# Kernel optimization log

Hardware: AMD Instinct MI355X
Metric: run time of the kernel (lower is better)

The kernel has to match this reference:

```python
import jax, jax.numpy as jnp
import numpy as np

N, D_IN = 40000, 3000
E = 640000
ALPHA = 0.9
BN_EPS = 0.001      # nn.BatchNorm in encoder/decoder blocks (eps=0.001)
BN_EPS_CONV = 1e-5  # PyG BatchNorm default eps
NEG_SLOPE = 0.2     # GATConv leaky_relu slope


def _bn(x, g, b, m, v, eps):
    # inference-mode batchnorm with running stats
    return (x - m) * (g / jnp.sqrt(v + eps)) + b


def _gat(h, src, dst, W, a_src, a_dst, bias, n):
    # PyG GATConv (heads=1): linear transform, per-edge additive attention,
    # segment softmax over incoming edges (self-loops already in src/dst).
    hw = h @ W                                   # [n, out]
    s_src = (hw * a_src).sum(-1)                 # [n]
    s_dst = (hw * a_dst).sum(-1)                 # [n]
    al = jax.nn.leaky_relu(s_src[src] + s_dst[dst], NEG_SLOPE)  # [e]
    mx = jax.ops.segment_max(al, dst, num_segments=n)
    e = jnp.exp(al - mx[dst])
    z = jax.ops.segment_sum(e, dst, num_segments=n)
    w = e / (z[dst] + 1e-16)                     # softmax weight per edge
    out = jax.ops.segment_sum(w[:, None] * hw[src], dst, num_segments=n)
    return out + bias


def _forward(x, edge_index,
             e0_w, e0_b, e0_g, e0_beta, e0_m, e0_v,
             e1_w, e1_b, e1_g, e1_beta, e1_m, e1_v,
             g1_w, g1_as, g1_ad, g1_b, bnc_g, bnc_beta, bnc_m, bnc_v,
             gm_w, gm_as, gm_ad, gm_b,
             gv_w, gv_as, gv_ad, gv_b,
             d0_w, d0_b, d0_g, d0_beta, d0_m, d0_v,
             out_w, out_b, cluster, eps):
    ar = jnp.arange(N, dtype=edge_index.dtype)
    src = jnp.concatenate([edge_index[0], ar])   # add self-loops (GATConv default)
    dst = jnp.concatenate([edge_index[1], ar])

    # linear encoder: Linear -> BN -> ELU (dropout inactive at eval)
    h = jax.nn.elu(_bn(x @ e0_w + e0_b, e0_g, e0_beta, e0_m, e0_v, BN_EPS))
    feat_x = jax.nn.elu(_bn(h @ e1_w + e1_b, e1_g, e1_beta, e1_m, e1_v, BN_EPS))

    # graph conv stack
    c = _gat(feat_x, src, dst, g1_w, g1_as, g1_ad, g1_b, N)
    c = jax.nn.relu(_bn(c, bnc_g, bnc_beta, bnc_m, bnc_v, BN_EPS_CONV))
    mu = _gat(c, src, dst, gm_w, gm_as, gm_ad, gm_b, N)
    logvar = _gat(c, src, dst, gv_w, gv_as, gv_ad, gv_b, N)

    # reparameterize (std = exp(logvar) per original code)
    gnn_z = eps * jnp.exp(logvar) + mu
    z = jnp.concatenate([feat_x, gnn_z], axis=1)  # [N, 28]

    # linear decoder
    d = jax.nn.elu(_bn(z @ d0_w + d0_b, d0_g, d0_beta, d0_m, d0_v, BN_EPS))
    de_feat = d @ out_w + out_b                   # [N, D_IN]

    # DEC student-t soft assignment (squared distance via expansion)
    sq = jnp.maximum(
        jnp.sum(z * z, 1)[:, None] + jnp.sum(cluster * cluster, 1)[None, :]
        - 2.0 * (z @ cluster.T), 0.0)             # [N, K]
    q = 1.0 / (1.0 + sq / ALPHA + 1e-8)
    q = q ** ((ALPHA + 1.0) / 2.0)
    q = q / jnp.sum(q, 1, keepdims=True)
    return z, mu, logvar, de_feat, q, feat_x, gnn_z


def setup_inputs() -> dict:
    key = jax.random.key(0)
    ks = iter(jax.random.split(key, 48))
    nrm = lambda shape, s=0.1: jax.random.normal(next(ks), shape, jnp.float32) * s
    pos = lambda shape: jax.random.uniform(next(ks), shape, jnp.float32, 0.5, 1.5)
    inp = {}
    inp['x'] = jax.random.normal(next(ks), (N, D_IN), jnp.float32)
    inp['edge_index'] = jax.random.randint(next(ks), (2, E), 0, N, jnp.int32)
    # encoder L0: 3000 -> 32
    inp.update(e0_w=nrm((D_IN, 32), 0.02), e0_b=nrm((32,)), e0_g=pos((32,)),
               e0_beta=nrm((32,)), e0_m=nrm((32,)), e0_v=pos((32,)))
    # encoder L1: 32 -> 20
    inp.update(e1_w=nrm((32, 20)), e1_b=nrm((20,)), e1_g=pos((20,)),
               e1_beta=nrm((20,)), e1_m=nrm((20,)), e1_v=pos((20,)))
    # GATConv 20 -> 64 (+ PyG BatchNorm)
    inp.update(g1_w=nrm((20, 64)), g1_as=nrm((64,)), g1_ad=nrm((64,)), g1_b=nrm((64,)),
               bnc_g=pos((64,)), bnc_beta=nrm((64,)), bnc_m=nrm((64,)), bnc_v=pos((64,)))
    # GATConv mean / logvar: 64 -> 8
    inp.update(gm_w=nrm((64, 8)), gm_as=nrm((8,)), gm_ad=nrm((8,)), gm_b=nrm((8,)))
    inp.update(gv_w=nrm((64, 8)), gv_as=nrm((8,)), gv_ad=nrm((8,)), gv_b=nrm((8,)))
    # decoder L0: 28 -> 32, out: 32 -> 3000
    inp.update(d0_w=nrm((28, 32)), d0_b=nrm((32,)), d0_g=pos((32,)),
               d0_beta=nrm((32,)), d0_m=nrm((32,)), d0_v=pos((32,)))
    inp.update(out_w=nrm((32, D_IN), 0.05), out_b=nrm((D_IN,)))
    inp['cluster'] = nrm((15, 28), 0.5)
    inp['eps'] = jax.random.normal(next(ks), (N, 8), jnp.float32)
    return inp


def reference(x, edge_index,
              e0_w, e0_b, e0_g, e0_beta, e0_m, e0_v,
              e1_w, e1_b, e1_g, e1_beta, e1_m, e1_v,
              g1_w, g1_as, g1_ad, g1_b, bnc_g, bnc_beta, bnc_m, bnc_v,
              gm_w, gm_as, gm_ad, gm_b,
              gv_w, gv_as, gv_ad, gv_b,
              d0_w, d0_b, d0_g, d0_beta, d0_m, d0_v,
              out_w, out_b, cluster, eps):
    return _forward(x, edge_index,
                    e0_w, e0_b, e0_g, e0_beta, e0_m, e0_v,
                    e1_w, e1_b, e1_g, e1_beta, e1_m, e1_v,
                    g1_w, g1_as, g1_ad, g1_b, bnc_g, bnc_beta, bnc_m, bnc_v,
                    gm_w, gm_as, gm_ad, gm_b,
                    gv_w, gv_as, gv_ad, gv_b,
                    d0_w, d0_b, d0_g, d0_beta, d0_m, d0_v,
                    out_w, out_b, cluster, eps)
```

## Files before the change

kernel.cpp:

```cpp
#include <hip/hip_runtime.h>
#include <cfloat>
#include <cmath>

#define NN 40000
#define DIN 3000
#define NE 640000
#define ET (NE + NN)

#define NKS 94
#define NKH 47
#define NCT 192
#define NB_E 2657
#define DCAP 64

typedef __attribute__((ext_vector_type(8))) short short8;
typedef __attribute__((ext_vector_type(4))) float f32x4;

union frag16 { short8 s; uint4 u; };

__device__ __forceinline__ float lrelu(float x) { return x >= 0.f ? x : 0.2f * x; }
__device__ __forceinline__ float elu(float x)   { return x > 0.f ? x : expm1f(x); }
__device__ __forceinline__ unsigned f2bf(float f) {
    unsigned u = __float_as_uint(f);
    return (u + 0x7FFFu + ((u >> 16) & 1u)) >> 16;
}
__device__ __forceinline__ float bf2f(unsigned short us) {
    return __uint_as_float((unsigned)us << 16);
}

__global__ void k_fill_prep(const int* __restrict__ ei, int* __restrict__ cnt,
                            int* __restrict__ srcs,
                            const float* __restrict__ w, const float* __restrict__ ow,
                            unsigned short* __restrict__ bfw,
                            unsigned short* __restrict__ bfragb)
{
    if (blockIdx.x < NB_E) {
        int e = blockIdx.x * 256 + threadIdx.x;
        if (e >= ET) return;
        int s, d;
        if (e < NE) { s = ei[e]; d = ei[NE + e]; } else { s = d = e - NE; }
        int pos = atomicAdd(&cnt[d], 1);
        if (pos < DCAP) srcs[((size_t)d << 6) + pos] = s;
    } else {
        int id = (blockIdx.x - NB_E) * 256 + threadIdx.x;
        if (id < 96 * 128) {
            int ks = id >> 7, r = id & 127;
            int t = r >> 6, l = r & 63;
            int col = t * 16 + (l & 15);
            int k0 = ks * 32 + ((l >> 4) << 3);
            unsigned v[8];
            #pragma unroll
            for (int j = 0; j < 8; j++) {
                int k = k0 + j;
                v[j] = (k < DIN) ? f2bf(w[(size_t)k * 32 + col]) : 0u;
            }
            uint4 p;
            p.x = v[0] | (v[1] << 16); p.y = v[2] | (v[3] << 16);
            p.z = v[4] | (v[5] << 16); p.w = v[6] | (v[7] << 16);
            *(uint4*)&bfw[(size_t)id * 8] = p;
        } else {
            int tt = id - 96 * 128;
            if (tt < NCT * 64) {
                int ct = tt >> 6, l = tt & 63;
                int col = ct * 16 + (l & 15);
                int k0 = (l >> 4) * 8;
                uint4 p = make_uint4(0u, 0u, 0u, 0u);
                if (col < DIN) {
                    unsigned v[8];
                    #pragma unroll
                    for (int j = 0; j < 8; j++)
                        v[j] = f2bf(ow[(size_t)(k0 + j) * DIN + col]);
                    p.x = v[0] | (v[1] << 16); p.y = v[2] | (v[3] << 16);
                    p.z = v[4] | (v[5] << 16); p.w = v[6] | (v[7] << 16);
                }
                *(uint4*)&bfragb[((size_t)ct * 64 + l) * 8] = p;
            }
        }
    }
}

__global__ __launch_bounds__(128) void k_enc0_prep(
    const float* __restrict__ x, const unsigned short* __restrict__ bfw,
    const float* __restrict__ b, const float* __restrict__ g,
    const float* __restrict__ beta, const float* __restrict__ m,
    const float* __restrict__ v,
    const float* __restrict__ e1w, const float* __restrict__ e1b,
    const float* __restrict__ e1g, const float* __restrict__ e1beta,
    const float* __restrict__ e1m, const float* __restrict__ e1v,
    const float* __restrict__ g1w, const float* __restrict__ g1as,
    const float* __restrict__ g1ad,
    float* __restrict__ out_fx, unsigned short* __restrict__ hw1b,
    float* __restrict__ s1src, float* __restrict__ s1dst)
{
    __shared__ float red[64 * 8];
    __shared__ float hs[16][33];
    __shared__ float fxs[16][20];
    const int tid = threadIdx.x, wid = tid >> 6, l = tid & 63;
    const int gg = blockIdx.x;
    const int row0 = gg * 16;
    const int row = row0 + (l & 15);
    const int klane = (l >> 4) << 3;

    const float* xp = x + (size_t)row * DIN + klane;
    const unsigned short* bp = bfw + (size_t)l * 8;

    f32x4 acc0 = {0.f, 0.f, 0.f, 0.f};
    f32x4 acc1 = {0.f, 0.f, 0.f, 0.f};

    const int ks0 = wid * NKH;
    #pragma unroll 4
    for (int ks = ks0; ks < ks0 + NKH; ks++) {
        frag16 a; a.u = make_uint4(0u, 0u, 0u, 0u);
        int k = ks * 32 + klane;
        if (k < DIN) {
            float4 v0 = *(const float4*)(xp + ks * 32);
            float4 v1 = *(const float4*)(xp + ks * 32 + 4);
            a.u.x = f2bf(v0.x) | (f2bf(v0.y) << 16);
            a.u.y = f2bf(v0.z) | (f2bf(v0.w) << 16);
            a.u.z = f2bf(v1.x) | (f2bf(v1.y) << 16);
            a.u.w = f2bf(v1.z) | (f2bf(v1.w) << 16);
        }
        frag16 b0, b1;
        b0.u = *(const uint4*)(bp + (size_t)(ks * 2 + 0) * 512);
        b1.u = *(const uint4*)(bp + (size_t)(ks * 2 + 1) * 512);
        acc0 = __builtin_amdgcn_mfma_f32_16x16x32_bf16(a.s, b0.s, acc0, 0, 0, 0);
        acc1 = __builtin_amdgcn_mfma_f32_16x16x32_bf16(a.s, b1.s, acc1, 0, 0, 0);
    }

    if (wid == 1) {
        #pragma unroll
        for (int r = 0; r < 4; r++) {
            red[l * 8 + r]     = acc0[r];
            red[l * 8 + 4 + r] = acc1[r];
        }
    }
    __syncthreads();
    if (wid == 0) {
        #pragma unroll
        for (int r = 0; r < 4; r++) {
            acc0[r] += red[l * 8 + r];
            acc1[r] += red[l * 8 + 4 + r];
        }
        const int cl = l & 15;
        const int rloc = (l >> 4) * 4;
        float sc0 = g[cl] * rsqrtf(v[cl] + 1e-3f);
        float sh0 = beta[cl] - m[cl] * sc0;
        float bb0 = b[cl];
        float sc1 = g[cl + 16] * rsqrtf(v[cl + 16] + 1e-3f);
        float sh1 = beta[cl + 16] - m[cl + 16] * sc1;
        float bb1 = b[cl + 16];
        #pragma unroll
        for (int reg = 0; reg < 4; reg++) {
            hs[rloc + reg][cl]      = elu((acc0[reg] + bb0) * sc0 + sh0);
            hs[rloc + reg][cl + 16] = elu((acc1[reg] + bb1) * sc1 + sh1);
        }
    }
    __syncthreads();

    for (int i = tid; i < 320; i += 128) {
        int r = i / 20, c = i - r * 20;
        float s = e1b[c];
        #pragma unroll
        for (int k = 0; k < 32; k++) s += hs[r][k] * e1w[k * 20 + c];
        float sc = e1g[c] * rsqrtf(e1v[c] + 1e-3f);
        s = (s - e1m[c]) * sc + e1beta[c];
        float fx = elu(s);
        fxs[r][c] = fx;
        out_fx[(size_t)(row0 + r) * 20 + c] = fx;
    }
    __syncthreads();

    #pragma unroll
    for (int j = 0; j < 8; j++) {
        const int rl = 2 * j + wid;
        float s = 0.f;
        #pragma unroll
        for (int k = 0; k < 20; k++) s += fxs[rl][k] * g1w[k * 64 + l];
        hw1b[(size_t)(row0 + rl) * 64 + l] = (unsigned short)f2bf(s);
        float u1 = s * g1as[l];
        float u2 = s * g1ad[l];
        u1 += __shfl_xor(u1, 1); u1 += __shfl_xor(u1, 2); u1 += __shfl_xor(u1, 4);
        u1 += __shfl_xor(u1, 8); u1 += __shfl_xor(u1, 16); u1 += __shfl_xor(u1, 32);
        u2 += __shfl_xor(u2, 1); u2 += __shfl_xor(u2, 2); u2 += __shfl_xor(u2, 4);
        u2 += __shfl_xor(u2, 8); u2 += __shfl_xor(u2, 16); u2 += __shfl_xor(u2, 32);
        if (l == 0) { s1src[row0 + rl] = u1; s1dst[row0 + rl] = u2; }
    }
}

__global__ __launch_bounds__(256) void k_gat1_fused(
    const int* __restrict__ cnt, const int* __restrict__ srcs,
    const float* __restrict__ s1src, const float* __restrict__ s1dst,
    const unsigned short* __restrict__ hw1b,
    const float* __restrict__ g1b,
    const float* __restrict__ bncg, const float* __restrict__ bncbeta,
    const float* __restrict__ bncm, const float* __restrict__ bncv,
    const float* __restrict__ gmw, const float* __restrict__ gmas, const float* __restrict__ gmad,
    const float* __restrict__ gvw, const float* __restrict__ gvas, const float* __restrict__ gvad,
    float* __restrict__ hwmv, float* __restrict__ sv4)
{
    __shared__ float cs[4][64];
    const int wv = threadIdx.x >> 6;
    int d = (blockIdx.x * 256 + threadIdx.x) >> 6;
    int l = threadIdx.x & 63;
    if (d >= NN) return;
    const int j0 = d << 6;
    int n = cnt[d]; n = (n < DCAP) ? n : DCAP;
    float sd = s1dst[d];
    float acc = 0.f, z = 0.f;
    int j = 0;
    for (; j + 4 <= n; j += 4) {
        int s0 = srcs[j0 + j], s1 = srcs[j0 + j + 1];
        int s2 = srcs[j0 + j + 2], s3 = srcs[j0 + j + 3];
        float a0 = s1src[s0], a1 = s1src[s1], a2 = s1src[s2], a3 = s1src[s3];
        float h0 = bf2f(hw1b[(size_t)s0 * 64 + l]);
        float h1 = bf2f(hw1b[(size_t)s1 * 64 + l]);
        float h2 = bf2f(hw1b[(size_t)s2 * 64 + l]);
        float h3 = bf2f(hw1b[(size_t)s3 * 64 + l]);
        float e0 = expf(lrelu(a0 + sd)), e1 = expf(lrelu(a1 + sd));
        float e2 = expf(lrelu(a2 + sd)), e3 = expf(lrelu(a3 + sd));
        z += (e0 + e1) + (e2 + e3);
        acc += e0 * h0; acc += e1 * h1; acc += e2 * h2; acc += e3 * h3;
    }
    for (; j < n; j++) {
        int s = srcs[j0 + j];
        float ex = expf(lrelu(s1src[s] + sd));
        z += ex;
        acc += ex * bf2f(hw1b[(size_t)s * 64 + l]);
    }
    float zi = 1.f / (z + 1e-16f);
    float val = acc * zi + g1b[l];
    float sc = bncg[l] * rsqrtf(bncv[l] + 1e-5f);
    val = (val - bncm[l]) * sc + bncbeta[l];
    float c = val > 0.f ? val : 0.f;
    cs[wv][l] = c;

    if (l < 16) {
        const bool isv = l >= 8;
        const int o = l & 7;
        const float* wmat = isv ? gvw : gmw;
        float s = 0.f;
        #pragma unroll 8
        for (int k = 0; k < 64; k++)
            s += cs[wv][k] * wmat[k * 8 + o];
        hwmv[(size_t)d * 16 + l] = s;
        float u1 = s * (isv ? gvas[o] : gmas[o]);
        float u2 = s * (isv ? gvad[o] : gmad[o]);
        u1 += __shfl_xor(u1, 1); u1 += __shfl_xor(u1, 2); u1 += __shfl_xor(u1, 4);
        u2 += __shfl_xor(u2, 1); u2 += __shfl_xor(u2, 2); u2 += __shfl_xor(u2, 4);
        if (o == 0) {
            if (!isv) { sv4[(size_t)d * 4 + 0] = u1; sv4[(size_t)d * 4 + 1] = u2; }
            else      { sv4[(size_t)d * 4 + 2] = u1; sv4[(size_t)d * 4 + 3] = u2; }
        }
    }
}

__global__ __launch_bounds__(256) void k_gat23_final(
    const int* __restrict__ cnt, const int* __restrict__ srcs,
    const float* __restrict__ hwmv, const float* __restrict__ sv4,
    const float* __restrict__ gmb, const float* __restrict__ gvb,
    const float* __restrict__ epsin, const float* __restrict__ fx_out,
    const float* __restrict__ d0w, const float* __restrict__ d0b,
    const float* __restrict__ d0g, const float* __restrict__ d0beta,
    const float* __restrict__ d0m, const float* __restrict__ d0v,
    const float* __restrict__ cluster,
    float* __restrict__ out_z, float* __restrict__ out_mu, float* __restrict__ out_lv,
    float* __restrict__ out_q, float* __restrict__ out_gz,
    unsigned short* __restrict__ abuf)
{
    __shared__ float zs[4][28];
    __shared__ float dvs[4][32];
    const int wv = threadIdx.x >> 6;
    int d = (blockIdx.x * 256 + threadIdx.x) >> 6;
    int l = threadIdx.x & 63;
    if (d >= NN) return;
    const int eg = l >> 4;
    const bool isv = (l & 15) >= 8;
    const int f = l & 7;
    const int fmv = l & 15;
    const int j0 = d << 6;
    int n = cnt[d]; n = (n < DCAP) ? n : DCAP;
    float sdst = sv4[(size_t)d * 4 + (isv ? 3 : 1)];
    float acc = 0.f, z = 0.f;
    for (int j = eg; j < n; j += 4) {
        int s = srcs[j0 + j];
        float a = sv4[(size_t)s * 4 + (isv ? 2 : 0)] + sdst;
        float ex = expf(lrelu(a));
        z += ex;
        acc += ex * hwmv[(size_t)s * 16 + fmv];
    }
    acc += __shfl_xor(acc, 16); acc += __shfl_xor(acc, 32);
    z   += __shfl_xor(z, 16);   z   += __shfl_xor(z, 32);
    float zi = 1.f / (z + 1e-16f);
    float t = acc * zi + (isv ? gvb[f] : gmb[f]);
    float partner = __shfl_xor(t, 8);
    float gz = 0.f;
    if (l < 8) gz = epsin[(size_t)d * 8 + f] * expf(partner) + t;
    if (l < 8)        { out_mu[(size_t)d * 8 + f] = t; out_gz[(size_t)d * 8 + f] = gz; }
    else if (l < 16)  { out_lv[(size_t)d * 8 + f] = t; }
    if (l < 20) zs[wv][l] = fx_out[(size_t)d * 20 + l];
    if (l < 8)  zs[wv][20 + l] = gz;
    if (l < 28) out_z[(size_t)d * 28 + l] = zs[wv][l];
    if (l < 32) {
        float s = d0b[l];
        #pragma unroll
        for (int k = 0; k < 28; k++) s += zs[wv][k] * d0w[k * 32 + l];
        float sc = d0g[l] * rsqrtf(d0v[l] + 1e-3f);
        s = (s - d0m[l]) * sc + d0beta[l];
        dvs[wv][l] = elu(s);
    }
    if (l < 4) {
        int g = d >> 4, rl = d & 15;
        const float* dv = dvs[wv];
        uint4 p;
        p.x = f2bf(dv[l*8+0]) | (f2bf(dv[l*8+1]) << 16);
        p.y = f2bf(dv[l*8+2]) | (f2bf(dv[l*8+3]) << 16);
        p.z = f2bf(dv[l*8+4]) | (f2bf(dv[l*8+5]) << 16);
        p.w = f2bf(dv[l*8+6]) | (f2bf(dv[l*8+7]) << 16);
        *(uint4*)&abuf[(size_t)g * 512 + (rl + 16 * l) * 8] = p;
    }
    float zz = 0.f;
    #pragma unroll
    for (int k = 0; k < 28; k++) { float zk = zs[wv][k]; zz += zk * zk; }
    float qb = 0.f;
    if (l < 15) {
        float cc = 0.f, zc = 0.f;
        #pragma unroll
        for (int k = 0; k < 28; k++) {
            float cv = cluster[l * 28 + k];
            cc += cv * cv; zc += zs[wv][k] * cv;
        }
        float sq = zz + cc - 2.f * zc;
        if (sq < 0.f) sq = 0.f;
        qb = 1.f / (1.f + sq * (1.f / 0.9f) + 1e-8f);
        qb = powf(qb, 0.95f);
    }
    float qs = qb;
    qs += __shfl_xor(qs, 1); qs += __shfl_xor(qs, 2);
    qs += __shfl_xor(qs, 4); qs += __shfl_xor(qs, 8);
    if (l < 15) out_q[(size_t)d * 15 + l] = qb / qs;
}

#define OTS 132
__global__ __launch_bounds__(256) void k_dec_out(
    const unsigned short* __restrict__ abuf, const unsigned short* __restrict__ bfragb,
    const float* __restrict__ ob, float* __restrict__ out_de)
{
    __shared__ float ot[64 * OTS];
    const int tid = threadIdx.x, wid = tid >> 6, l = tid & 63;
    const int gblk = blockIdx.y;
    const int ct0 = blockIdx.x * 8;
    frag16 a; a.u = *(const uint4*)&abuf[((size_t)(gblk * 4 + wid)) * 512 + l * 8];
    const int lrow = wid * 16 + (l >> 4) * 4;
    const int cl = l & 15;
    #pragma unroll
    for (int c = 0; c < 8; c++) {
        frag16 bfr; bfr.u = *(const uint4*)&bfragb[((size_t)(ct0 + c) * 64 + l) * 8];
        f32x4 acc = {0.f, 0.f, 0.f, 0.f};
        acc = __builtin_amdgcn_mfma_f32_16x16x32_bf16(a.s, bfr.s, acc, 0, 0, 0);
        #pragma unroll
        for (int reg = 0; reg < 4; reg++)
            ot[(lrow + reg) * OTS + c * 16 + cl] = acc[reg];
    }
    __syncthreads();
    const int row0 = gblk * 64;
    const int c0 = ct0 * 16;
    #pragma unroll
    for (int i = 0; i < 8; i++) {
        int idx = i * 256 + tid;
        int r = idx >> 5, q = idx & 31;
        int col = c0 + q * 4;
        if (col < DIN) {
            const float* p = &ot[r * OTS + q * 4];
            float4 bq = *(const float4*)&ob[col];
            f32x4 o;
            o[0] = p[0] + bq.x; o[1] = p[1] + bq.y;
            o[2] = p[2] + bq.z; o[3] = p[3] + bq.w;
            __builtin_nontemporal_store(o, (f32x4*)&out_de[(size_t)(row0 + r) * DIN + col]);
        }
    }
}

extern "C" void kernel_launch(void* const* d_in, const int* in_sizes, int n_in,
                              void* d_out, int out_size, void* d_ws, size_t ws_size,
                              hipStream_t stream) {
    const float* x      = (const float*)d_in[0];
    const int*   ei     = (const int*)  d_in[1];
    const float* e0_w   = (const float*)d_in[2];
    const float* e0_b   = (const float*)d_in[3];
    const float* e0_g   = (const float*)d_in[4];
    const float* e0_be  = (const float*)d_in[5];
    const float* e0_m   = (const float*)d_in[6];
    const float* e0_v   = (const float*)d_in[7];
    const float* e1_w   = (const float*)d_in[8];
    const float* e1_b   = (const float*)d_in[9];
    const float* e1_g   = (const float*)d_in[10];
    const float* e1_be  = (const float*)d_in[11];
    const float* e1_m   = (const float*)d_in[12];
    const float* e1_v   = (const float*)d_in[13];
    const float* g1_w   = (const float*)d_in[14];
    const float* g1_as  = (const float*)d_in[15];
    const float* g1_ad  = (const float*)d_in[16];
    const float* g1_b   = (const float*)d_in[17];
    const float* bnc_g  = (const float*)d_in[18];
    const float* bnc_be = (const float*)d_in[19];
    const float* bnc_m  = (const float*)d_in[20];
    const float* bnc_v  = (const float*)d_in[21];
    const float* gm_w   = (const float*)d_in[22];
    const float* gm_as  = (const float*)d_in[23];
    const float* gm_ad  = (const float*)d_in[24];
    const float* gm_b   = (const float*)d_in[25];
    const float* gv_w   = (const float*)d_in[26];
    const float* gv_as  = (const float*)d_in[27];
    const float* gv_ad  = (const float*)d_in[28];
    const float* gv_b   = (const float*)d_in[29];
    const float* d0_w   = (const float*)d_in[30];
    const float* d0_b   = (const float*)d_in[31];
    const float* d0_g   = (const float*)d_in[32];
    const float* d0_be  = (const float*)d_in[33];
    const float* d0_m   = (const float*)d_in[34];
    const float* d0_v   = (const float*)d_in[35];
    const float* out_w  = (const float*)d_in[36];
    const float* out_b  = (const float*)d_in[37];
    const float* cluster= (const float*)d_in[38];
    const float* epsin  = (const float*)d_in[39];

    float* out = (float*)d_out;
    float* out_z  = out;
    float* out_mu = out + (size_t)NN * 28;
    float* out_lv = out + (size_t)NN * 36;
    float* out_de = out + (size_t)NN * 44;
    float* out_q  = out + (size_t)NN * 44 + (size_t)NN * DIN;
    float* out_fx = out + (size_t)NN * 59 + (size_t)NN * DIN;
    float* out_gz = out + (size_t)NN * 79 + (size_t)NN * DIN;

    float* ws = (float*)d_ws;
    const size_t n = NN;
    unsigned short* hw1b = (unsigned short*)(ws + 64 * n);
    float* s1src   = ws + 96 * n;
    float* s1dst   = ws + 97 * n;
    unsigned short* abuf   = (unsigned short*)(ws + 103 * n);
    unsigned short* bfw    = (unsigned short*)(ws + 119 * n);
    unsigned short* bfragb = (unsigned short*)(ws + 121 * n);
    float* hwmv = ws;
    float* sv4  = ws + 16 * n;

    int* srcs = (int*)out_de;
    int* cnt  = srcs + (size_t)NN * DCAP;

    const int NB_PREP = (96 * 128 + NCT * 64 + 255) / 256;

    (void)hipMemsetAsync(cnt, 0, NN * sizeof(int), stream);
    k_fill_prep<<<NB_E + NB_PREP, 256, 0, stream>>>(ei, cnt, srcs, e0_w, out_w, bfw, bfragb);

    k_enc0_prep<<<NN / 16, 128, 0, stream>>>(x, bfw, e0_b, e0_g, e0_be, e0_m, e0_v,
                                             e1_w, e1_b, e1_g, e1_be, e1_m, e1_v,
                                             g1_w, g1_as, g1_ad,
                                             out_fx, hw1b, s1src, s1dst);
    k_gat1_fused<<<(NN * 64 + 255) / 256, 256, 0, stream>>>(cnt, srcs,
                                                            s1src, s1dst, hw1b,
                                                            g1_b, bnc_g, bnc_be, bnc_m, bnc_v,
                                                            gm_w, gm_as, gm_ad,
                                                            gv_w, gv_as, gv_ad,
                                                            hwmv, sv4);
    k_gat23_final<<<(NN * 64 + 255) / 256, 256, 0, stream>>>(cnt, srcs,
                                                             hwmv, sv4,
                                                             gm_b, gv_b, epsin, out_fx,
                                                             d0_w, d0_b, d0_g, d0_be, d0_m, d0_v,
                                                             cluster,
                                                             out_z, out_mu, out_lv, out_q, out_gz,
                                                             abuf);
    dim3 dec_grid(NCT / 8, NN / 64);
    k_dec_out<<<dec_grid, 256, 0, stream>>>(abuf, bfragb, out_b, out_de);
}
```

Baseline: 433.0 us.

## Move edge bucketing into encoder kernel to overlap with the GEMM

The edge-to-destination bucketing (atomic count plus source scatter) moves out of the weight-prep kernel and into the front of the encoder GEMM kernel's grid, using extra blocks. The weight-prep kernel now only converts weights to bf16 fragments and launches far fewer blocks. The aim is to run the latency-bound atomic scatter alongside the bandwidth-bound x@W encoder instead of serially before it. The extra scatter blocks are dispatched first and could delay the GEMM blocks.

```diff
diff --git a/kernel.cpp b/kernel.cpp
--- a/kernel.cpp
+++ b/kernel.cpp
@@ -28,53 +28,42 @@
     return __uint_as_float((unsigned)us << 16);
 }
 
-__global__ void k_fill_prep(const int* __restrict__ ei, int* __restrict__ cnt,
-                            int* __restrict__ srcs,
-                            const float* __restrict__ w, const float* __restrict__ ow,
-                            unsigned short* __restrict__ bfw,
-                            unsigned short* __restrict__ bfragb)
+__global__ void k_wprep(const float* __restrict__ w, const float* __restrict__ ow,
+                        unsigned short* __restrict__ bfw,
+                        unsigned short* __restrict__ bfragb)
 {
-    if (blockIdx.x < NB_E) {
-        int e = blockIdx.x * 256 + threadIdx.x;
-        if (e >= ET) return;
-        int s, d;
-        if (e < NE) { s = ei[e]; d = ei[NE + e]; } else { s = d = e - NE; }
-        int pos = atomicAdd(&cnt[d], 1);
-        if (pos < DCAP) srcs[((size_t)d << 6) + pos] = s;
+    int id = blockIdx.x * 256 + threadIdx.x;
+    if (id < 96 * 128) {
+        int ks = id >> 7, r = id & 127;
+        int t = r >> 6, l = r & 63;
+        int col = t * 16 + (l & 15);
+        int k0 = ks * 32 + ((l >> 4) << 3);
+        unsigned v[8];
+        #pragma unroll
+        for (int j = 0; j < 8; j++) {
+            int k = k0 + j;
+            v[j] = (k < DIN) ? f2bf(w[(size_t)k * 32 + col]) : 0u;
+        }
+        uint4 p;
+        p.x = v[0] | (v[1] << 16); p.y = v[2] | (v[3] << 16);
+        p.z = v[4] | (v[5] << 16); p.w = v[6] | (v[7] << 16);
+        *(uint4*)&bfw[(size_t)id * 8] = p;
     } else {
-        int id = (blockIdx.x - NB_E) * 256 + threadIdx.x;
-        if (id < 96 * 128) {
-            int ks = id >> 7, r = id & 127;
-            int t = r >> 6, l = r & 63;
-            int col = t * 16 + (l & 15);
-            int k0 = ks * 32 + ((l >> 4) << 3);
-            unsigned v[8];
-            #pragma unroll
-            for (int j = 0; j < 8; j++) {
-                int k = k0 + j;
-                v[j] = (k < DIN) ? f2bf(w[(size_t)k * 32 + col]) : 0u;
+        int tt = id - 96 * 128;
+        if (tt < NCT * 64) {
+            int ct = tt >> 6, l = tt & 63;
+            int col = ct * 16 + (l & 15);
+            int k0 = (l >> 4) * 8;
+            uint4 p = make_uint4(0u, 0u, 0u, 0u);
+            if (col < DIN) {
+                unsigned v[8];
+                #pragma unroll
+                for (int j = 0; j < 8; j++)
+                    v[j] = f2bf(ow[(size_t)(k0 + j) * DIN + col]);
+                p.x = v[0] | (v[1] << 16); p.y = v[2] | (v[3] << 16);
+                p.z = v[4] | (v[5] << 16); p.w = v[6] | (v[7] << 16);
             }
-            uint4 p;
-            p.x = v[0] | (v[1] << 16); p.y = v[2] | (v[3] << 16);
-            p.z = v[4] | (v[5] << 16); p.w = v[6] | (v[7] << 16);
-            *(uint4*)&bfw[(size_t)id * 8] = p;
-        } else {
-            int tt = id - 96 * 128;
-            if (tt < NCT * 64) {
-                int ct = tt >> 6, l = tt & 63;
-                int col = ct * 16 + (l & 15);
-                int k0 = (l >> 4) * 8;
-                uint4 p = make_uint4(0u, 0u, 0u, 0u);
-                if (col < DIN) {
-                    unsigned v[8];
-                    #pragma unroll
-                    for (int j = 0; j < 8; j++)
-                        v[j] = f2bf(ow[(size_t)(k0 + j) * DIN + col]);
-                    p.x = v[0] | (v[1] << 16); p.y = v[2] | (v[3] << 16);
-                    p.z = v[4] | (v[5] << 16); p.w = v[6] | (v[7] << 16);
-                }
-                *(uint4*)&bfragb[((size_t)ct * 64 + l) * 8] = p;
-            }
+            *(uint4*)&bfragb[((size_t)ct * 64 + l) * 8] = p;
         }
     }
 }
@@ -90,13 +79,31 @@
     const float* __restrict__ g1w, const float* __restrict__ g1as,
     const float* __restrict__ g1ad,
     float* __restrict__ out_fx, unsigned short* __restrict__ hw1b,
-    float* __restrict__ s1src, float* __restrict__ s1dst)
+    float* __restrict__ s1src, float* __restrict__ s1dst,
+    const int* __restrict__ ei, int* __restrict__ cnt, int* __restrict__ srcs)
 {
+    const int tid = threadIdx.x;
+    if (blockIdx.x < NB_E) {
+        int e = blockIdx.x * 128 + (tid & 127);
+        #pragma unroll
+        for (int half = 0; half < 2; half++) {
+            int ee = blockIdx.x * 256 + half * 128 + tid;
+            if (ee < ET) {
+                int s, d;
+                if (ee < NE) { s = ei[ee]; d = ei[NE + ee]; } else { s = d = ee - NE; }
+                int pos = atomicAdd(&cnt[d], 1);
+                if (pos < DCAP) srcs[((size_t)d << 6) + pos] = s;
+            }
+        }
+        (void)e;
+        return;
+    }
+
     __shared__ float red[64 * 8];
     __shared__ float hs[16][33];
     __shared__ float fxs[16][20];
-    const int tid = threadIdx.x, wid = tid >> 6, l = tid & 63;
-    const int gg = blockIdx.x;
+    const int wid = tid >> 6, l = tid & 63;
+    const int gg = blockIdx.x - NB_E;
     const int row0 = gg * 16;
     const int row = row0 + (l & 15);
     const int klane = (l >> 4) << 3;
@@ -450,12 +457,13 @@
     const int NB_PREP = (96 * 128 + NCT * 64 + 255) / 256;
 
     (void)hipMemsetAsync(cnt, 0, NN * sizeof(int), stream);
-    k_fill_prep<<<NB_E + NB_PREP, 256, 0, stream>>>(ei, cnt, srcs, e0_w, out_w, bfw, bfragb);
-
-    k_enc0_prep<<<NN / 16, 128, 0, stream>>>(x, bfw, e0_b, e0_g, e0_be, e0_m, e0_v,
-                                             e1_w, e1_b, e1_g, e1_be, e1_m, e1_v,
-                                             g1_w, g1_as, g1_ad,
-                                             out_fx, hw1b, s1src, s1dst);
+    k_wprep<<<NB_PREP, 256, 0, stream>>>(e0_w, out_w, bfw, bfragb);
+
+    k_enc0_prep<<<NB_E + NN / 16, 128, 0, stream>>>(x, bfw, e0_b, e0_g, e0_be, e0_m, e0_v,
+                                                    e1_w, e1_b, e1_g, e1_be, e1_m, e1_v,
+                                                    g1_w, g1_as, g1_ad,
+                                                    out_fx, hw1b, s1src, s1dst,
+                                                    ei, cnt, srcs);
     k_gat1_fused<<<(NN * 64 + 255) / 256, 256, 0, stream>>>(cnt, srcs,
                                                             s1src, s1dst, hw1b,
                                                             g1_b, bnc_g, bnc_be, bnc_m, bnc_v,
```

Result: slower. 471.8 us (+8.9%).
